# Kernel optimization log

Measured on AMD Instinct MI355X. Metric: run time of the kernel, lower is better.

Reference implementation:

```python
import jax, jax.numpy as jnp
import numpy as np

B, T, F, H = 1024, 512, 40, 50


def setup_inputs() -> dict:
    key = jax.random.key(0)
    ks = jax.random.split(key, 9)
    s = 0.1
    return {
        "x": jax.random.normal(ks[0], (B, T, F), dtype=jnp.float32),
        "W_ih": jax.random.normal(ks[1], (4 * H, F), dtype=jnp.float32) * s,
        "W_hh": jax.random.normal(ks[2], (4 * H, H), dtype=jnp.float32) * s,
        "b_ih": jax.random.normal(ks[3], (4 * H,), dtype=jnp.float32) * s,
        "b_hh": jax.random.normal(ks[4], (4 * H,), dtype=jnp.float32) * s,
        "W1": jax.random.normal(ks[5], (10, H), dtype=jnp.float32) * s,
        "b1": jax.random.normal(ks[6], (10,), dtype=jnp.float32) * s,
        "W2": jax.random.normal(ks[7], (1, 10), dtype=jnp.float32) * s,
        "b2": jax.random.normal(ks[8], (1,), dtype=jnp.float32) * s,
    }


def reference(x, W_ih, W_hh, b_ih, b_hh, W1, b1, W2, b2):
    b, t, f = x.shape
    h = W_hh.shape[1]
    # Precompute input projections for all timesteps: [T, B, 4H]
    xg = jnp.einsum("btf,gf->tbg", x, W_ih) + (b_ih + b_hh)

    h0 = jnp.zeros((b, h), dtype=x.dtype)
    c0 = jnp.zeros((b, h), dtype=x.dtype).at[:, 0].set(1.0)

    def step(carry, xg_t):
        hx, cx = carry
        gates = xg_t + hx @ W_hh.T  # [B, 4H]
        i, fg, g, o = jnp.split(gates, 4, axis=-1)  # PyTorch gate order i,f,g,o
        i = jax.nn.sigmoid(i)
        fg = jax.nn.sigmoid(fg)
        g = jnp.tanh(g)
        o = jax.nn.sigmoid(o)
        cx = fg * cx + i * g
        hx = o * jnp.tanh(cx)
        return (hx, cx), None

    (hx, _), _ = jax.lax.scan(step, (h0, c0), xg)
    head = jax.nn.relu(hx @ W1.T + b1) @ W2.T + b2  # [B, 1]
    return head + x[:, -1, 0:1]
```

## Files before the change

kernel.cpp:

```cpp
#include <hip/hip_runtime.h>


constexpr int kT   = 512;
constexpr int kF   = 40;
constexpr int kH   = 50;
constexpr int kMB  = 2;
constexpr int kRowS = 104;
constexpr int kGRow = 208;

typedef __attribute__((ext_vector_type(8))) short bf16x8;
typedef __attribute__((ext_vector_type(4))) float f32x4;

__device__ __forceinline__ unsigned short f2bf(float f) {
    union { float f; unsigned u; } v; v.f = f;
    return (unsigned short)((v.u + 0x7FFFu + ((v.u >> 16) & 1u)) >> 16);
}
__device__ __forceinline__ float fast_sigmoid(float v) {
    return __builtin_amdgcn_rcpf(1.f + __expf(-v));
}
__device__ __forceinline__ float fast_tanh(float v) {
    return 1.f - 2.f * __builtin_amdgcn_rcpf(__expf(2.f * v) + 1.f);
}

__global__ __launch_bounds__(256, 2)
void lstm_mfma_2cu(
    const float* __restrict__ x,
    const float* __restrict__ W_ih,
    const float* __restrict__ W_hh,
    const float* __restrict__ b_ih,
    const float* __restrict__ b_hh,
    const float* __restrict__ W1,
    const float* __restrict__ b1,
    const float* __restrict__ W2,
    const float* __restrict__ b2,
    float* __restrict__ out)
{
    const int tid  = threadIdx.x;
    const int lane = tid & 63;
    const int wave = tid >> 6;
    const int bb   = blockIdx.x;
    const int m16  = lane & 15;
    const int q    = lane >> 4;

    __shared__ short sh_comb[2][16][kRowS];
    __shared__ float sh_g[kMB][kGRow];
    __shared__ float sh_hf[kMB][kH + 2];
    __shared__ float sh_head[kMB][10];

    const int t0 = (wave == 3) ? 9 : wave * 3;
    const int NT = (wave == 3) ? 4 : 3;

    { int* z = (int*)sh_comb; for (int i = tid; i < 1664; i += 256) z[i] = 0; }

    bf16x8 wa[4][3];
    float  bias[4][4];
    const int uA = m16 >> 2, gA = m16 & 3;
#pragma unroll
    for (int i = 0; i < 4; ++i) {
        const int tl = t0 + i;
        const int unitA = 4 * tl + uA;
        const bool live = (i < NT) && (unitA < kH);
        const int orow = live ? (unitA + 50 * gA) : 0;
#pragma unroll
        for (int kk = 0; kk < 3; ++kk) {
            bf16x8 v;
#pragma unroll
            for (int j = 0; j < 8; ++j) {
                const int k = kk * 32 + q * 8 + j;
                float wv = 0.f;
                if (live) {
                    if (k < kF)           wv = W_ih[orow * kF + k];
                    else if (k < kF + kH) wv = W_hh[orow * kH + (k - kF)];
                }
                v[j] = (short)f2bf(wv);
            }
            wa[i][kk] = v;
        }
        const int uD = 4 * tl + q;
#pragma unroll
        for (int r = 0; r < 4; ++r)
            bias[i][r] = (i < NT && uD < kH)
                       ? (b_ih[uD + 50 * r] + b_hh[uD + 50 * r]) : 0.f;
    }

    const bool pw = (tid < kMB * kH);
    const int  pm = pw ? (tid / kH) : 0;
    const int  pu = pw ? (tid % kH) : 0;
    float c     = (pw && pu == 0) ? 1.f : 0.f;
    float lasth = 0.f;

    const bool xs = (tid >= 128 && tid < 128 + kMB * 20);
    const int  xi = xs ? (tid - 128) : 0;
    const int  xm = xi / 20, xd = xi % 20;
    const float* xrow = x + ((size_t)(bb * kMB + xm) * kT) * kF + 2 * xd;

    float2 pa = {0.f, 0.f}, pb = {0.f, 0.f};
    __syncthreads();
    if (xs) {
        float2 v0 = *(const float2*)xrow;
        unsigned pk = (unsigned)f2bf(v0.x) | ((unsigned)f2bf(v0.y) << 16);
        *(unsigned*)&sh_comb[0][xm][2 * xd] = pk;
        pa = *(const float2*)(xrow + (size_t)1 * kF);
        pb = *(const float2*)(xrow + (size_t)2 * kF);
    }
    __syncthreads();

    auto step = [&](int t, int CUR, float2& pf) {
        const short* rowp = &sh_comb[CUR][m16][0];
        bf16x8 bv0 = *(const bf16x8*)(rowp +      q * 8);
        bf16x8 bv1 = *(const bf16x8*)(rowp + 32 + q * 8);
        bf16x8 bv2 = *(const bf16x8*)(rowp + 64 + q * 8);
#pragma unroll
        for (int i = 0; i < 4; ++i) {
            if (i < NT) {
                f32x4 d;
                d[0] = bias[i][0]; d[1] = bias[i][1];
                d[2] = bias[i][2]; d[3] = bias[i][3];
                d = __builtin_amdgcn_mfma_f32_16x16x32_bf16(wa[i][0], bv0, d, 0, 0, 0);
                d = __builtin_amdgcn_mfma_f32_16x16x32_bf16(wa[i][1], bv1, d, 0, 0, 0);
                d = __builtin_amdgcn_mfma_f32_16x16x32_bf16(wa[i][2], bv2, d, 0, 0, 0);
                if (m16 < kMB)
                    *(f32x4*)&sh_g[m16][16 * (t0 + i) + 4 * q] = d;
            }
        }
        __syncthreads();

        short* nbuf = &sh_comb[CUR ^ 1][0][0];
        if (pw) {
            f32x4 g = *(const f32x4*)&sh_g[pm][4 * pu];
            float i_s = fast_sigmoid(g[0]);
            float f_s = fast_sigmoid(g[1]);
            float g_t = fast_tanh   (g[2]);
            float o_s = fast_sigmoid(g[3]);
            c = fmaf(f_s, c, i_s * g_t);
            lasth = o_s * fast_tanh(c);
            if (t + 1 < kT)
                nbuf[pm * kRowS + kF + pu] = (short)f2bf(lasth);
        } else if (xs) {
            if (t + 1 < kT) {
                unsigned pk = (unsigned)f2bf(pf.x) | ((unsigned)f2bf(pf.y) << 16);
                *(unsigned*)&nbuf[xm * kRowS + 2 * xd] = pk;
            }
            if (t + 3 < kT)
                pf = *(const float2*)(xrow + (size_t)(t + 3) * kF);
        }
        __syncthreads();
    };

    for (int t = 0; t < kT; t += 2) {
        step(t,     0, pa);
        step(t + 1, 1, pb);
    }

    if (pw) sh_hf[pm][pu] = lasth;
    __syncthreads();
    if (tid < kMB * 10) {
        const int m = tid / 10, j = tid % 10;
        float acc = b1[j];
#pragma unroll
        for (int k = 0; k < kH; ++k) acc = fmaf(sh_hf[m][k], W1[j * kH + k], acc);
        sh_head[m][j] = fmaxf(acc, 0.f);
    }
    __syncthreads();
    if (tid < kMB) {
        float acc = b2[0];
#pragma unroll
        for (int j2 = 0; j2 < 10; ++j2) acc = fmaf(sh_head[tid][j2], W2[j2], acc);
        const int bidx = bb * kMB + tid;
        out[bidx] = acc + x[((size_t)bidx * kT + (kT - 1)) * kF];
    }
}

extern "C" void kernel_launch(void* const* d_in, const int* in_sizes, int n_in,
                              void* d_out, int out_size, void* d_ws, size_t ws_size,
                              hipStream_t stream) {
    const float* x    = (const float*)d_in[0];
    const float* W_ih = (const float*)d_in[1];
    const float* W_hh = (const float*)d_in[2];
    const float* b_ih = (const float*)d_in[3];
    const float* b_hh = (const float*)d_in[4];
    const float* W1   = (const float*)d_in[5];
    const float* b1   = (const float*)d_in[6];
    const float* W2   = (const float*)d_in[7];
    const float* b2   = (const float*)d_in[8];
    float* out = (float*)d_out;

    lstm_mfma_2cu<<<dim3(1024 / kMB), dim3(256), 0, stream>>>(
        x, W_ih, W_hh, b_ih, b_hh, W1, b1, W2, b2, out);
}
```

Measured before the change: 359.3 us.

## Stage x input in 16-timestep chunks with float4 prefetch into ring buffer

Result: slower. 381.4 us (+6.2%).

```diff
diff --git a/kernel.cpp b/kernel.cpp
--- a/kernel.cpp
+++ b/kernel.cpp
@@ -1,14 +1,15 @@
 #include <hip/hip_runtime.h>
 
 
-constexpr int kT   = 512;
-constexpr int kF   = 40;
-constexpr int kH   = 50;
-constexpr int kMB  = 2;
+constexpr int kT  = 512;
+constexpr int kF  = 40;
+constexpr int kH  = 50;
+constexpr int kMB = 2;
+constexpr int kCH = 16;
 constexpr int kRowS = 104;
-constexpr int kGRow = 208;
 
 typedef __attribute__((ext_vector_type(8))) short bf16x8;
+typedef __attribute__((ext_vector_type(4))) short short4v;
 typedef __attribute__((ext_vector_type(4))) float f32x4;
 
 __device__ __forceinline__ unsigned short f2bf(float f) {
@@ -23,7 +24,7 @@
 }
 
 __global__ __launch_bounds__(256, 2)
-void lstm_mfma_2cu(
+void lstm_mfma_r9(
     const float* __restrict__ x,
     const float* __restrict__ W_ih,
     const float* __restrict__ W_hh,
@@ -42,9 +43,9 @@
     const int m16  = lane & 15;
     const int q    = lane >> 4;
 
-    __shared__ short sh_comb[2][16][kRowS];
-    __shared__ float sh_g[kMB][kGRow];
-    __shared__ float sh_hf[kMB][kH + 2];
+    __shared__ short sh_comb[kCH][kMB][kRowS];
+    __shared__ float sh_g[kMB][13 * 16];
+    __shared__ float sh_hf[kMB][52];
     __shared__ float sh_head[kMB][10];
 
     const int t0 = (wave == 3) ? 9 : wave * 3;
@@ -69,8 +70,8 @@
                 const int k = kk * 32 + q * 8 + j;
                 float wv = 0.f;
                 if (live) {
-                    if (k < kF)           wv = W_ih[orow * kF + k];
-                    else if (k < kF + kH) wv = W_hh[orow * kH + (k - kF)];
+                    if (k < kF)                     wv = W_ih[orow * kF + k];
+                    else if (k < kF + kH)           wv = W_hh[orow * kH + (k - kF)];
                 }
                 v[j] = (short)f2bf(wv);
             }
@@ -89,27 +90,55 @@
     float c     = (pw && pu == 0) ? 1.f : 0.f;
     float lasth = 0.f;
 
-    const bool xs = (tid >= 128 && tid < 128 + kMB * 20);
-    const int  xi = xs ? (tid - 128) : 0;
-    const int  xm = xi / 20, xd = xi % 20;
-    const float* xrow = x + ((size_t)(bb * kMB + xm) * kT) * kF + 2 * xd;
-
-    float2 pa = {0.f, 0.f}, pb = {0.f, 0.f};
-    __syncthreads();
-    if (xs) {
-        float2 v0 = *(const float2*)xrow;
-        unsigned pk = (unsigned)f2bf(v0.x) | ((unsigned)f2bf(v0.y) << 16);
-        *(unsigned*)&sh_comb[0][xm][2 * xd] = pk;
-        pa = *(const float2*)(xrow + (size_t)1 * kF);
-        pb = *(const float2*)(xrow + (size_t)2 * kF);
-    }
-    __syncthreads();
-
-    auto step = [&](int t, int CUR, float2& pf) {
-        const short* rowp = &sh_comb[CUR][m16][0];
+    float4 pf[2];
+    const int idx1 = tid + 256;
+#pragma unroll
+    for (int r = 0; r < 2; ++r) {
+        const int idx = tid + 256 * r;
+        if (idx < 320) {
+            const int m = idx / 160, rem = idx % 160;
+            const int ts = rem / 10, fi = rem % 10;
+            pf[r] = *(const float4*)(
+                x + ((size_t)(bb * kMB + m) * kT + ts) * kF + 4 * fi);
+        }
+    }
+
+    for (int t = 0; t < kT; ++t) {
+        const int tc = t & (kCH - 1);
+
+        if (tc == 0) {
+#pragma unroll
+            for (int r = 0; r < 2; ++r) {
+                const int idx = tid + 256 * r;
+                if (idx < 320) {
+                    const int m = idx / 160, rem = idx % 160;
+                    const int ts = rem / 10, fi = rem % 10;
+                    short4v s;
+                    s[0] = (short)f2bf(pf[r].x); s[1] = (short)f2bf(pf[r].y);
+                    s[2] = (short)f2bf(pf[r].z); s[3] = (short)f2bf(pf[r].w);
+                    *(short4v*)&sh_comb[ts][m][4 * fi] = s;
+                }
+            }
+            __syncthreads();
+            if (t + kCH < kT) {
+#pragma unroll
+                for (int r = 0; r < 2; ++r) {
+                    const int idx = tid + 256 * r;
+                    if (idx < 320) {
+                        const int m = idx / 160, rem = idx % 160;
+                        const int ts = rem / 10, fi = rem % 10;
+                        pf[r] = *(const float4*)(
+                            x + ((size_t)(bb * kMB + m) * kT + (t + kCH + ts)) * kF + 4 * fi);
+                    }
+                }
+            }
+        }
+
+        const short* rowp = &sh_comb[tc][m16 & 1][0];
         bf16x8 bv0 = *(const bf16x8*)(rowp +      q * 8);
         bf16x8 bv1 = *(const bf16x8*)(rowp + 32 + q * 8);
         bf16x8 bv2 = *(const bf16x8*)(rowp + 64 + q * 8);
+
 #pragma unroll
         for (int i = 0; i < 4; ++i) {
             if (i < NT) {
@@ -125,7 +154,6 @@
         }
         __syncthreads();
 
-        short* nbuf = &sh_comb[CUR ^ 1][0][0];
         if (pw) {
             f32x4 g = *(const f32x4*)&sh_g[pm][4 * pu];
             float i_s = fast_sigmoid(g[0]);
@@ -134,22 +162,9 @@
             float o_s = fast_sigmoid(g[3]);
             c = fmaf(f_s, c, i_s * g_t);
             lasth = o_s * fast_tanh(c);
-            if (t + 1 < kT)
-                nbuf[pm * kRowS + kF + pu] = (short)f2bf(lasth);
-        } else if (xs) {
-            if (t + 1 < kT) {
-                unsigned pk = (unsigned)f2bf(pf.x) | ((unsigned)f2bf(pf.y) << 16);
-                *(unsigned*)&nbuf[xm * kRowS + 2 * xd] = pk;
-            }
-            if (t + 3 < kT)
-                pf = *(const float2*)(xrow + (size_t)(t + 3) * kF);
+            sh_comb[(t + 1) & (kCH - 1)][pm][kF + pu] = (short)f2bf(lasth);
         }
         __syncthreads();
-    };
-
-    for (int t = 0; t < kT; t += 2) {
-        step(t,     0, pa);
-        step(t + 1, 1, pb);
     }
 
     if (pw) sh_hf[pm][pu] = lasth;
@@ -185,6 +200,6 @@
     const float* b2   = (const float*)d_in[8];
     float* out = (float*)d_out;
 
-    lstm_mfma_2cu<<<dim3(1024 / kMB), dim3(256), 0, stream>>>(
+    lstm_mfma_r9<<<dim3(1024 / kMB), dim3(256), 0, stream>>>(
         x, W_ih, W_hh, b_ih, b_hh, W1, b1, W2, b2, out);
 }
```
